# Kernel optimization log

Hardware: AMD Instinct MI355X
Metric: run time of the kernel (lower is better)

Reference implementation:

```python
import jax, jax.numpy as jnp
import numpy as np


def _ln(x, g, b, eps=1e-5):
    m = x.mean(-1, keepdims=True)
    v = ((x - m) ** 2).mean(-1, keepdims=True)
    return (x - m) * jax.lax.rsqrt(v + eps) * g + b


def setup_inputs() -> dict:
    key = jax.random.key(0)
    ks = jax.random.split(key, 12)
    B, S, I, H, E, P, O, EM = 32, 512, 64, 512, 8, 96, 64, 512
    D = S * I
    r = lambda k, shape, s=0.02: jax.random.normal(k, shape, jnp.float32) * s
    z = lambda *shape: jnp.zeros(shape, jnp.float32)
    o = lambda *shape: jnp.ones(shape, jnp.float32)
    return dict(
        x=jax.random.normal(ks[0], (B, S, I), jnp.float32),
        gW1=r(ks[1], (D, EM)), gb1=z(EM), gln1_g=o(EM), gln1_b=z(EM),
        gW2=r(ks[2], (EM, EM)), gb2=z(EM), gln2_g=o(EM), gln2_b=z(EM),
        gW3=r(ks[3], (EM, 128)), gb3=z(128),
        protos=jax.random.normal(ks[4], (E, 128), jnp.float32) * 0.01,
        temp=jnp.ones((), jnp.float32),
        eW1=r(ks[5], (E, I, H)), eb1=z(E, H),
        eW2=r(ks[6], (E, H, H)), eb2=z(E, H),
        fW1=r(ks[7], (H, H)), fb1=z(H), fln_g=o(H), fln_b=z(H),
        fW2=r(ks[8], (H, H)), fb2=z(H),
        ln_g=o(H), ln_b=z(H),
        pW1=r(ks[9], (H, H // 2)), pb1=z(H // 2), pln_g=o(H // 2), pln_b=z(H // 2),
        pW2=r(ks[10], (H // 2, P * O)), pb2=z(P * O),
        on_g=o(O), on_b=z(O),
    )


def reference(x, gW1, gb1, gln1_g, gln1_b, gW2, gb2, gln2_g, gln2_b, gW3, gb3,
              protos, temp, eW1, eb1, eW2, eb2,
              fW1, fb1, fln_g, fln_b, fW2, fb2, ln_g, ln_b,
              pW1, pb1, pln_g, pln_b, pW2, pb2, on_g, on_b):
    B, S, I = x.shape
    O = on_g.shape[0]
    P = pW2.shape[1] // O
    # 1) flow latent mapping (identity fallback path of the original code)
    x_flat = x.reshape(B, S * I)
    z_latent = x_flat
    # 2) gating encoder -> 128-d embedding (dropout = identity in eval)
    h = jax.nn.relu(_ln(z_latent @ gW1 + gb1, gln1_g, gln1_b))
    h = jax.nn.relu(_ln(h @ gW2 + gb2, gln2_g, gln2_b))
    emb = h @ gW3 + gb3  # [B, 128]
    # 3) routing: euclidean cdist to prototypes, temperature-scaled softmax
    d2 = jnp.sum((emb[:, None, :] - protos[None, :, :]) ** 2, axis=-1)
    dist = jnp.sqrt(jnp.maximum(d2, 1e-12))  # [B, E]
    t = jnp.clip(temp, 0.1, 5.0)
    w = jax.nn.softmax(-dist / t, axis=-1)  # [B, E]
    # 4) experts: per-expert FFN on raw input, all experts batched
    he = jax.nn.relu(jnp.einsum('bsi,eih->besh', x, eW1) + eb1[None, :, None, :])
    eo = jnp.einsum('besh,eho->beso', he, eW2) + eb2[None, :, None, :]  # [B,E,S,H]
    # 5) routing-weighted combine + fusion + prediction head
    fused = jnp.einsum('besh,be->bsh', eo, w)
    f = jax.nn.relu(_ln(fused @ fW1 + fb1, fln_g, fln_b)) @ fW2 + fb2
    f = _ln(f, ln_g, ln_b)
    last = f[:, -1, :]  # [B, H]
    p = jax.nn.relu(_ln(last @ pW1 + pb1, pln_g, pln_b)) @ pW2 + pb2
    p = p.reshape(B, P, O)
    return _ln(p, on_g, on_b)
```

## Files before the change

kernel.cpp:

```cpp
#include <hip/hip_runtime.h>
#include <math.h>

#define DIMK 32768

__device__ __forceinline__ void fma4(float4& a, float s, const float4 w) {
  a.x += s * w.x; a.y += s * w.y; a.z += s * w.z; a.w += s * w.w;
}

__device__ __forceinline__ float fsel(const float4& v, int kk) {
  return kk == 0 ? v.x : kk == 1 ? v.y : kk == 2 ? v.z : v.w;
}

__device__ __forceinline__ float wave_sum(float v) {
  v += __shfl_xor(v, 1); v += __shfl_xor(v, 2); v += __shfl_xor(v, 4);
  v += __shfl_xor(v, 8); v += __shfl_xor(v, 16); v += __shfl_xor(v, 32);
  return v;
}

__device__ __forceinline__ void gld_lds16(const float* g, float* l) {
  __builtin_amdgcn_global_load_lds(
      (const __attribute__((address_space(1))) void*)g,
      (__attribute__((address_space(3))) void*)l, 16, 0, 0);
}

__device__ __forceinline__ float block_sum(float v, float* red, int n) {
  int t = threadIdx.x;
  red[t] = v;
  __syncthreads();
  for (int s = n >> 1; s > 0; s >>= 1) {
    if (t < s) red[t] += red[t + s];
    __syncthreads();
  }
  float r = red[0];
  __syncthreads();
  return r;
}

__global__ __launch_bounds__(256) void gemm1(const float* __restrict__ x,
                                             const float* __restrict__ gW1,
                                             float* __restrict__ part) {
  const int mt = blockIdx.x, ks = blockIdx.y;
  const int m0 = mt * 128, k0 = ks * 256;
  const int t = threadIdx.x;
  __shared__ float As[32 * 256];
  __shared__ float Ws[2][32 * 128];

  const float* Wp = gW1 + (size_t)k0 * 512 + m0;

#pragma unroll
  for (int j = 0; j < 8; ++j) {
    int i = t + j * 256;
    gld_lds16(x + (size_t)(i >> 6) * DIMK + k0 + (i & 63) * 4, &As[i * 4]);
  }
#pragma unroll
  for (int j = 0; j < 4; ++j) {
    int i = t + j * 256;
    gld_lds16(Wp + (size_t)(i >> 5) * 512 + (i & 31) * 4, &Ws[0][i * 4]);
  }

  const int mf4 = (t & 31) * 4;
  const int bg = t >> 5;
  float4 acc[4];
#pragma unroll
  for (int j = 0; j < 4; ++j) acc[j] = make_float4(0.f, 0.f, 0.f, 0.f);
  const float* a0 = &As[bg * 4 * 256];

  for (int s = 0; s < 8; ++s) {
    __syncthreads();
    if (s < 7) {
      const float* Wn = Wp + (size_t)(s + 1) * 32 * 512;
#pragma unroll
      for (int j = 0; j < 4; ++j) {
        int i = t + j * 256;
        gld_lds16(Wn + (size_t)(i >> 5) * 512 + (i & 31) * 4, &Ws[(s + 1) & 1][i * 4]);
      }
    }
    const float* Wc = Ws[s & 1];
    const int sc = s * 32;
#pragma unroll
    for (int kq = 0; kq < 8; ++kq) {
      float4 av0 = *(const float4*)(a0 + sc + kq * 4);
      float4 av1 = *(const float4*)(a0 + 256 + sc + kq * 4);
      float4 av2 = *(const float4*)(a0 + 512 + sc + kq * 4);
      float4 av3 = *(const float4*)(a0 + 768 + sc + kq * 4);
#pragma unroll
      for (int kk = 0; kk < 4; ++kk) {
        float4 wv = *(const float4*)&Wc[(kq * 4 + kk) * 128 + mf4];
        fma4(acc[0], fsel(av0, kk), wv);
        fma4(acc[1], fsel(av1, kk), wv);
        fma4(acc[2], fsel(av2, kk), wv);
        fma4(acc[3], fsel(av3, kk), wv);
      }
    }
  }

  float* op = part + ((size_t)ks * 32 + bg * 4) * 512 + m0 + mf4;
#pragma unroll
  for (int j = 0; j < 4; ++j) *(float4*)(op + (size_t)j * 512) = acc[j];
}

__global__ __launch_bounds__(256) void pr_he(const float* __restrict__ part,
                                             float* __restrict__ pre,
                                             const float* __restrict__ x,
                                             const float* __restrict__ eW1,
                                             const float* __restrict__ eb1,
                                             float* __restrict__ he_all) {
  __shared__ float sm[18432];
  const int bid = blockIdx.x, t = threadIdx.x;
  if (bid < 256) {
    const int b = bid & 31, c = bid >> 5;
#pragma unroll
    for (int h = 0; h < 2; ++h) {
      int m = t + h * 256;
      float a = 0.f;
      const float* p = part + ((size_t)c * 16 * 32 + b) * 512 + m;
#pragma unroll
      for (int i = 0; i < 16; ++i) a += p[(size_t)i * 16384];
      pre[((size_t)c * 32 + b) * 512 + m] = a;
    }
  } else {
    const int idx = bid - 256;
    const int e = idx >> 1, hs = idx & 1;
    float* xs = sm;
    float* Ws = sm + 2048;
    for (int i = t; i < 512; i += 256) {
      int b = i >> 4, q = i & 15;
      *(float4*)&xs[b * 64 + q * 4] = *(const float4*)(x + (size_t)b * DIMK + 32704 + q * 4);
    }
    const float* w1 = eW1 + (size_t)e * 64 * 512 + hs * 256;
    for (int i = t; i < 64 * 64; i += 256) {
      int k = i >> 6, q = i & 63;
      *(float4*)&Ws[k * 256 + q * 4] = *(const float4*)(w1 + (size_t)k * 512 + q * 4);
    }
    __syncthreads();
    float acc[32];
#pragma unroll
    for (int b = 0; b < 32; ++b) acc[b] = 0.f;
#pragma unroll 4
    for (int k = 0; k < 64; ++k) {
      float wk = Ws[k * 256 + t];
#pragma unroll
      for (int b = 0; b < 32; ++b) acc[b] += xs[b * 64 + k] * wk;
    }
    float bb = eb1[e * 512 + hs * 256 + t];
    for (int b = 0; b < 32; ++b)
      he_all[((size_t)e * 32 + b) * 512 + hs * 256 + t] = fmaxf(acc[b] + bb, 0.f);
  }
}

__global__ __launch_bounds__(256) void ln_eg(const float* __restrict__ pre,
                                             const float* __restrict__ gb1,
                                             const float* __restrict__ g,
                                             const float* __restrict__ bt,
                                             float* __restrict__ h1,
                                             const float* __restrict__ he_all,
                                             const float* __restrict__ eW2,
                                             float* __restrict__ epart) {
  __shared__ float sm[6272];
  const int bid = blockIdx.x, t = threadIdx.x;
  if (bid < 32) {
    const int b = bid;
    float a0 = gb1[t], a1 = gb1[t + 256];
    for (int kq = 0; kq < 8; ++kq) {
      const float* p = pre + ((size_t)kq * 32 + b) * 512;
      a0 += p[t]; a1 += p[t + 256];
    }
    const int lane = t & 63, wid = t >> 6;
    float s = wave_sum(a0 + a1);
    if (lane == 0) sm[wid] = s;
    __syncthreads();
    float mean = (sm[0] + sm[1] + sm[2] + sm[3]) * (1.f / 512.f);
    float d0 = a0 - mean, d1 = a1 - mean;
    __syncthreads();
    float q = wave_sum(d0 * d0 + d1 * d1);
    if (lane == 0) sm[wid] = q;
    __syncthreads();
    float var = (sm[0] + sm[1] + sm[2] + sm[3]) * (1.f / 512.f);
    float rr = rsqrtf(var + 1e-5f);
    h1[b * 512 + t] = fmaxf(d0 * rr * g[t] + bt[t], 0.f);
    h1[b * 512 + t + 256] = fmaxf(d1 * rr * g[t + 256] + bt[t + 256], 0.f);
  } else {
    const int idx = bid - 32;
    const int mt = idx & 7, kq = (idx >> 3) & 7, e = idx >> 6;
    constexpr int KC = 64;
    float* Ws = sm;
    float* As = sm + KC * 64;
    const int m0 = mt * 64, k0 = kq * KC;
    const float* Wp = eW2 + (size_t)e * 512 * 512 + (size_t)k0 * 512 + m0;
    for (int i = t; i < KC * 16; i += 256) {
      int r = i >> 4, q = i & 15;
      *(float4*)&Ws[r * 64 + q * 4] = *(const float4*)(Wp + (size_t)r * 512 + q * 4);
    }
    const float* Ap = he_all + (size_t)e * 32 * 512 + k0;
    for (int i = t; i < 32 * (KC / 4); i += 256) {
      int b = i / (KC / 4), q = i % (KC / 4);
      *(float4*)&As[b * (KC + 4) + q * 4] = *(const float4*)(Ap + (size_t)b * 512 + q * 4);
    }
    __syncthreads();
    const int mf = t & 15, bg = t >> 4;
    const int b0 = bg * 2;
    float4 acc0 = make_float4(0.f, 0.f, 0.f, 0.f), acc1 = acc0;
    const float* a0 = &As[b0 * (KC + 4)];
    const float* a1 = &As[(b0 + 1) * (KC + 4)];
#pragma unroll 8
    for (int k = 0; k < KC; ++k) {
      float4 wv = *(const float4*)&Ws[k * 64 + mf * 4];
      fma4(acc0, a0[k], wv);
      fma4(acc1, a1[k], wv);
    }
    float* op = epart + ((size_t)(kq * 8 + e) * 32 + b0) * 512 + m0 + mf * 4;
    *(float4*)op = acc0;
    *(float4*)(op + 512) = acc1;
  }
}

template <int KC>
__global__ __launch_bounds__(256) void gemm_tile(const float* __restrict__ A,
                                                 const float* __restrict__ W,
                                                 float* __restrict__ outp,
                                                 int M, int aRow) {
  const int mt = blockIdx.x, kq = blockIdx.y;
  const int m0 = mt * 64, k0 = kq * KC;
  const int t = threadIdx.x;
  __shared__ float Ws[KC * 64];
  __shared__ float As[32 * (KC + 4)];
  const float* Wp = W + (size_t)k0 * M + m0;
  for (int i = t; i < KC * 16; i += 256) {
    int r = i >> 4, q = i & 15;
    *(float4*)&Ws[r * 64 + q * 4] = *(const float4*)(Wp + (size_t)r * M + q * 4);
  }
  const float* Ap = A + k0;
  for (int i = t; i < 32 * (KC / 4); i += 256) {
    int b = i / (KC / 4), q = i % (KC / 4);
    *(float4*)&As[b * (KC + 4) + q * 4] = *(const float4*)(Ap + (size_t)b * aRow + q * 4);
  }
  __syncthreads();
  const int mf = t & 15, bg = t >> 4;
  const int b0 = bg * 2;
  float4 acc0 = make_float4(0.f, 0.f, 0.f, 0.f), acc1 = acc0;
  const float* a0 = &As[b0 * (KC + 4)];
  const float* a1 = &As[(b0 + 1) * (KC + 4)];
#pragma unroll 8
  for (int k = 0; k < KC; ++k) {
    float4 wv = *(const float4*)&Ws[k * 64 + mf * 4];
    fma4(acc0, a0[k], wv);
    fma4(acc1, a1[k], wv);
  }
  float* op = outp + ((size_t)kq * 32 + b0) * M + m0 + mf * 4;
  *(float4*)op = acc0;
  *(float4*)(op + M) = acc1;
}

__global__ void red_ln(const float* __restrict__ zp, const float* __restrict__ bias,
                       const float* __restrict__ g, const float* __restrict__ bt,
                       float* __restrict__ outp, int M, int nq, int relu) {
  const int b = blockIdx.x, t = threadIdx.x;
  __shared__ float red[512];
  float a = bias[t];
#pragma unroll 4
  for (int kq = 0; kq < nq; ++kq) a += zp[((size_t)kq * 32 + b) * M + t];
  float fM = 1.f / (float)M;
  float mean = block_sum(a, red, M) * fM;
  float d = a - mean;
  float var = block_sum(d * d, red, M) * fM;
  float v = d * rsqrtf(var + 1e-5f) * g[t] + bt[t];
  outp[b * M + t] = relu ? fmaxf(v, 0.f) : v;
}

__global__ __launch_bounds__(512) void gate_mix(const float* __restrict__ zp,
                                                const float* __restrict__ gb2,
                                                const float* __restrict__ g2,
                                                const float* __restrict__ bt2,
                                                const float* __restrict__ gW3,
                                                const float* __restrict__ gb3,
                                                const float* __restrict__ protos,
                                                const float* __restrict__ temp,
                                                const float* __restrict__ epart,
                                                const float* __restrict__ eb2,
                                                float* __restrict__ fused) {
  const int b = blockIdx.x, t = threadIdx.x;
  __shared__ float red[512];
  __shared__ float Arow[512];
  __shared__ float pacc[16 * 128];
  __shared__ float emb[128];
  __shared__ float d2s[8];
  __shared__ float wl[8];

  float a = gb2[t];
#pragma unroll
  for (int kq = 0; kq < 8; ++kq) a += zp[((size_t)kq * 32 + b) * 512 + t];
  float mean = block_sum(a, red, 512) * (1.f / 512.f);
  float d = a - mean;
  float var = block_sum(d * d, red, 512) * (1.f / 512.f);
  Arow[t] = fmaxf(d * rsqrtf(var + 1e-5f) * g2[t] + bt2[t], 0.f);
  __syncthreads();

  const int m4 = (t & 31) * 4, kg = t >> 5;
  const float* Wp = gW3 + (size_t)kg * 32 * 128 + m4;
  float4 acc = make_float4(0.f, 0.f, 0.f, 0.f);
  const float* ar = &Arow[kg * 32];
#pragma unroll 8
  for (int k = 0; k < 32; ++k) {
    float4 wv = *(const float4*)(Wp + (size_t)k * 128);
    fma4(acc, ar[k], wv);
  }
  *(float4*)&pacc[kg * 128 + m4] = acc;
  __syncthreads();
  if (t < 128) {
    float e = gb3[t];
#pragma unroll
    for (int k2 = 0; k2 < 16; ++k2) e += pacc[k2 * 128 + t];
    emb[t] = e;
  }
  __syncthreads();

  const int lane = t & 63, wid = t >> 6;
  float dd0 = emb[lane] - protos[wid * 128 + lane];
  float dd1 = emb[lane + 64] - protos[wid * 128 + 64 + lane];
  float q = wave_sum(dd0 * dd0 + dd1 * dd1);
  if (lane == 0) d2s[wid] = q;
  __syncthreads();
  if (t == 0) {
    float tt = fminf(fmaxf(temp[0], 0.1f), 5.0f);
    float lg[8], mx = -1e30f;
#pragma unroll
    for (int e = 0; e < 8; ++e) {
      float dist = sqrtf(fmaxf(d2s[e], 1e-12f));
      lg[e] = -dist / tt;
      mx = fmaxf(mx, lg[e]);
    }
    float se = 0.f;
#pragma unroll
    for (int e = 0; e < 8; ++e) { lg[e] = expf(lg[e] - mx); se += lg[e]; }
#pragma unroll
    for (int e = 0; e < 8; ++e) wl[e] = lg[e] / se;
  }
  __syncthreads();

  float fa = 0.f;
#pragma unroll
  for (int e = 0; e < 8; ++e) {
    float s = eb2[e * 512 + t];
#pragma unroll
    for (int kq = 0; kq < 8; ++kq)
      s += epart[(((size_t)kq * 8 + e) * 32 + b) * 512 + t];
    fa += wl[e] * s;
  }
  fused[b * 512 + t] = fa;
}

__global__ __launch_bounds__(256) void fin_red(const float* __restrict__ fpart,
                                               const float* __restrict__ pb2,
                                               const float* __restrict__ ong,
                                               const float* __restrict__ onb,
                                               float* __restrict__ outp) {
  const int t = threadIdx.x;
  const int lane = t & 63, w = t >> 6;
  const int r = blockIdx.x * 4 + w;
  const int b = r / 96, pi = r % 96;
  const int m = pi * 64 + lane;
  float a = pb2[m];
#pragma unroll
  for (int kq = 0; kq < 4; ++kq) a += fpart[((size_t)kq * 32 + b) * 6144 + m];
  float s = wave_sum(a);
  float mean = s * (1.f / 64.f);
  float d = a - mean;
  float q = wave_sum(d * d);
  float rr = rsqrtf(q * (1.f / 64.f) + 1e-5f);
  outp[((size_t)b * 96 + pi) * 64 + lane] = d * rr * ong[lane] + onb[lane];
}

extern "C" void kernel_launch(void* const* d_in, const int* in_sizes, int n_in,
                              void* d_out, int out_size, void* d_ws, size_t ws_size,
                              hipStream_t stream) {
  (void)in_sizes; (void)n_in; (void)out_size; (void)ws_size;
  const float* x      = (const float*)d_in[0];
  const float* gW1    = (const float*)d_in[1];
  const float* gb1    = (const float*)d_in[2];
  const float* gln1_g = (const float*)d_in[3];
  const float* gln1_b = (const float*)d_in[4];
  const float* gW2    = (const float*)d_in[5];
  const float* gb2    = (const float*)d_in[6];
  const float* gln2_g = (const float*)d_in[7];
  const float* gln2_b = (const float*)d_in[8];
  const float* gW3    = (const float*)d_in[9];
  const float* gb3    = (const float*)d_in[10];
  const float* protos = (const float*)d_in[11];
  const float* temp   = (const float*)d_in[12];
  const float* eW1    = (const float*)d_in[13];
  const float* eb1    = (const float*)d_in[14];
  const float* eW2    = (const float*)d_in[15];
  const float* eb2    = (const float*)d_in[16];
  const float* fW1    = (const float*)d_in[17];
  const float* fb1    = (const float*)d_in[18];
  const float* fln_g  = (const float*)d_in[19];
  const float* fln_b  = (const float*)d_in[20];
  const float* fW2    = (const float*)d_in[21];
  const float* fb2    = (const float*)d_in[22];
  const float* ln_g   = (const float*)d_in[23];
  const float* ln_b   = (const float*)d_in[24];
  const float* pW1    = (const float*)d_in[25];
  const float* pb1    = (const float*)d_in[26];
  const float* pln_g  = (const float*)d_in[27];
  const float* pln_b  = (const float*)d_in[28];
  const float* pW2    = (const float*)d_in[29];
  const float* pb2    = (const float*)d_in[30];
  const float* on_g   = (const float*)d_in[31];
  const float* on_b   = (const float*)d_in[32];
  float* out = (float*)d_out;

  float* ws     = (float*)d_ws;
  float* part   = ws;
  float* epart  = ws;
  float* he_all = ws + 1048576;
  float* fpart  = ws;
  float* h1     = ws + 2097152;
  float* zp     = h1 + 16384;
  float* fused  = zp + 262144;
  float* f1     = fused + 16384;
  float* lastv  = f1 + 16384;
  float* pp     = lastv + 16384;

  gemm1<<<dim3(4, 128), 256, 0, stream>>>(x, gW1, part);
  pr_he<<<272, 256, 0, stream>>>(part, zp, x, eW1, eb1, he_all);
  ln_eg<<<544, 256, 0, stream>>>(zp, gb1, gln1_g, gln1_b, h1, he_all, eW2, epart);
  gemm_tile<64><<<dim3(8, 8), 256, 0, stream>>>(h1, gW2, zp, 512, 512);
  gate_mix<<<32, 512, 0, stream>>>(zp, gb2, gln2_g, gln2_b, gW3, gb3, protos,
                                   temp, epart, eb2, fused);
  gemm_tile<64><<<dim3(8, 8), 256, 0, stream>>>(fused, fW1, zp, 512, 512);
  red_ln<<<32, 512, 0, stream>>>(zp, fb1, fln_g, fln_b, f1, 512, 8, 1);
  gemm_tile<64><<<dim3(8, 8), 256, 0, stream>>>(f1, fW2, zp, 512, 512);
  red_ln<<<32, 512, 0, stream>>>(zp, fb2, ln_g, ln_b, lastv, 512, 8, 0);
  gemm_tile<64><<<dim3(4, 8), 256, 0, stream>>>(lastv, pW1, zp, 256, 512);
  red_ln<<<32, 256, 0, stream>>>(zp, pb1, pln_g, pln_b, pp, 256, 8, 1);
  gemm_tile<64><<<dim3(96, 4), 256, 0, stream>>>(pp, pW2, fpart, 6144, 256);
  fin_red<<<768, 256, 0, stream>>>(fpart, pb2, on_g, on_b, out);
}
```

Before: 273.1 us.

## Split gate_mix into 4 column chunks per batch and use wave-level reductions

Replaces the tree-based shared-memory block_sum in red_ln with wave shuffles plus a small per-wave cross-sum, cutting the number of barriers. The gate/mix kernel is relaunched as a 32x4 grid of 128-thread blocks. Each block redundantly recomputes the LN, the gW3 projection and the softmax routing, then handles only a 128-column slice of the expert combine. This spreads the heavy epart read across four times more blocks, at the cost of repeating the gating work four times with a serial 512-length dot per thread.

Result: slower. 293.4 us (+7.4%).

```diff
diff --git a/kernel.cpp b/kernel.cpp
--- a/kernel.cpp
+++ b/kernel.cpp
@@ -17,23 +17,16 @@
   return v;
 }
 
+__device__ __forceinline__ float group16_sum(float v) {
+  v += __shfl_xor(v, 1); v += __shfl_xor(v, 2);
+  v += __shfl_xor(v, 4); v += __shfl_xor(v, 8);
+  return v;
+}
+
 __device__ __forceinline__ void gld_lds16(const float* g, float* l) {
   __builtin_amdgcn_global_load_lds(
       (const __attribute__((address_space(1))) void*)g,
       (__attribute__((address_space(3))) void*)l, 16, 0, 0);
-}
-
-__device__ __forceinline__ float block_sum(float v, float* red, int n) {
-  int t = threadIdx.x;
-  red[t] = v;
-  __syncthreads();
-  for (int s = n >> 1; s > 0; s >>= 1) {
-    if (t < s) red[t] += red[t + s];
-    __syncthreads();
-  }
-  float r = red[0];
-  __syncthreads();
-  return r;
 }
 
 __global__ __launch_bounds__(256) void gemm1(const float* __restrict__ x,
@@ -255,70 +248,98 @@
                        const float* __restrict__ g, const float* __restrict__ bt,
                        float* __restrict__ outp, int M, int nq, int relu) {
   const int b = blockIdx.x, t = threadIdx.x;
-  __shared__ float red[512];
+  __shared__ float red[8];
+  const int nw = M >> 6;
   float a = bias[t];
 #pragma unroll 4
   for (int kq = 0; kq < nq; ++kq) a += zp[((size_t)kq * 32 + b) * M + t];
+  const int lane = t & 63, wid = t >> 6;
   float fM = 1.f / (float)M;
-  float mean = block_sum(a, red, M) * fM;
+  float s = wave_sum(a);
+  if (lane == 0) red[wid] = s;
+  __syncthreads();
+  float tot = 0.f;
+  for (int w = 0; w < nw; ++w) tot += red[w];
+  float mean = tot * fM;
   float d = a - mean;
-  float var = block_sum(d * d, red, M) * fM;
+  __syncthreads();
+  float q = wave_sum(d * d);
+  if (lane == 0) red[wid] = q;
+  __syncthreads();
+  float tv = 0.f;
+  for (int w = 0; w < nw; ++w) tv += red[w];
+  float var = tv * fM;
   float v = d * rsqrtf(var + 1e-5f) * g[t] + bt[t];
   outp[b * M + t] = relu ? fmaxf(v, 0.f) : v;
 }
 
-__global__ __launch_bounds__(512) void gate_mix(const float* __restrict__ zp,
-                                                const float* __restrict__ gb2,
-                                                const float* __restrict__ g2,
-                                                const float* __restrict__ bt2,
-                                                const float* __restrict__ gW3,
-                                                const float* __restrict__ gb3,
-                                                const float* __restrict__ protos,
-                                                const float* __restrict__ temp,
-                                                const float* __restrict__ epart,
-                                                const float* __restrict__ eb2,
-                                                float* __restrict__ fused) {
-  const int b = blockIdx.x, t = threadIdx.x;
-  __shared__ float red[512];
+__global__ __launch_bounds__(128) void ffuse_gate(const float* __restrict__ zp,
+                                                  const float* __restrict__ gb2,
+                                                  const float* __restrict__ g2,
+                                                  const float* __restrict__ bt2,
+                                                  const float* __restrict__ gW3,
+                                                  const float* __restrict__ gb3,
+                                                  const float* __restrict__ protos,
+                                                  const float* __restrict__ temp,
+                                                  const float* __restrict__ epart,
+                                                  const float* __restrict__ eb2,
+                                                  float* __restrict__ fused) {
+  const int b = blockIdx.x, ch = blockIdx.y, t = threadIdx.x;
   __shared__ float Arow[512];
-  __shared__ float pacc[16 * 128];
   __shared__ float emb[128];
+  __shared__ float red2[2];
   __shared__ float d2s[8];
   __shared__ float wl[8];
 
-  float a = gb2[t];
-#pragma unroll
-  for (int kq = 0; kq < 8; ++kq) a += zp[((size_t)kq * 32 + b) * 512 + t];
-  float mean = block_sum(a, red, 512) * (1.f / 512.f);
-  float d = a - mean;
-  float var = block_sum(d * d, red, 512) * (1.f / 512.f);
-  Arow[t] = fmaxf(d * rsqrtf(var + 1e-5f) * g2[t] + bt2[t], 0.f);
-  __syncthreads();
-
-  const int m4 = (t & 31) * 4, kg = t >> 5;
-  const float* Wp = gW3 + (size_t)kg * 32 * 128 + m4;
-  float4 acc = make_float4(0.f, 0.f, 0.f, 0.f);
-  const float* ar = &Arow[kg * 32];
+  float a[4];
+#pragma unroll
+  for (int j = 0; j < 4; ++j) {
+    int m = t + j * 128;
+    float v = gb2[m];
+#pragma unroll
+    for (int kq = 0; kq < 8; ++kq) v += zp[((size_t)kq * 32 + b) * 512 + m];
+    a[j] = v;
+  }
+  const int lane = t & 63, wid = t >> 6;
+  float s = wave_sum(a[0] + a[1] + a[2] + a[3]);
+  if (lane == 0) red2[wid] = s;
+  __syncthreads();
+  float mean = (red2[0] + red2[1]) * (1.f / 512.f);
+  float q = 0.f;
+#pragma unroll
+  for (int j = 0; j < 4; ++j) { float d = a[j] - mean; q += d * d; }
+  __syncthreads();
+  q = wave_sum(q);
+  if (lane == 0) red2[wid] = q;
+  __syncthreads();
+  float rr = rsqrtf((red2[0] + red2[1]) * (1.f / 512.f) + 1e-5f);
+#pragma unroll
+  for (int j = 0; j < 4; ++j) {
+    int m = t + j * 128;
+    Arow[m] = fmaxf((a[j] - mean) * rr * g2[m] + bt2[m], 0.f);
+  }
+  __syncthreads();
+
+  {
+    float e = gb3[t];
 #pragma unroll 8
-  for (int k = 0; k < 32; ++k) {
-    float4 wv = *(const float4*)(Wp + (size_t)k * 128);
-    fma4(acc, ar[k], wv);
-  }
-  *(float4*)&pacc[kg * 128 + m4] = acc;
-  __syncthreads();
-  if (t < 128) {
-    float e = gb3[t];
-#pragma unroll
-    for (int k2 = 0; k2 < 16; ++k2) e += pacc[k2 * 128 + t];
+    for (int k = 0; k < 512; ++k) e += Arow[k] * gW3[(size_t)k * 128 + t];
     emb[t] = e;
   }
   __syncthreads();
 
-  const int lane = t & 63, wid = t >> 6;
-  float dd0 = emb[lane] - protos[wid * 128 + lane];
-  float dd1 = emb[lane + 64] - protos[wid * 128 + 64 + lane];
-  float q = wave_sum(dd0 * dd0 + dd1 * dd1);
-  if (lane == 0) d2s[wid] = q;
+  {
+    const int e = t >> 4, l16 = t & 15;
+    float qq = 0.f;
+#pragma unroll
+    for (int j = 0; j < 8; ++j) {
+      int dix = l16 + j * 16;
+      float dd = emb[dix] - protos[e * 128 + dix];
+      qq += dd * dd;
+    }
+    qq = group16_sum(qq);
+    if (l16 == 0) d2s[e] = qq;
+  }
   __syncthreads();
   if (t == 0) {
     float tt = fminf(fmaxf(temp[0], 0.1f), 5.0f);
@@ -337,16 +358,17 @@
   }
   __syncthreads();
 
+  const int m = ch * 128 + t;
   float fa = 0.f;
 #pragma unroll
   for (int e = 0; e < 8; ++e) {
-    float s = eb2[e * 512 + t];
+    float se = eb2[e * 512 + m];
 #pragma unroll
     for (int kq = 0; kq < 8; ++kq)
-      s += epart[(((size_t)kq * 8 + e) * 32 + b) * 512 + t];
-    fa += wl[e] * s;
-  }
-  fused[b * 512 + t] = fa;
+      se += epart[(((size_t)kq * 8 + e) * 32 + b) * 512 + m];
+    fa += wl[e] * se;
+  }
+  fused[b * 512 + m] = fa;
 }
 
 __global__ __launch_bounds__(256) void fin_red(const float* __restrict__ fpart,
@@ -425,8 +447,8 @@
   pr_he<<<272, 256, 0, stream>>>(part, zp, x, eW1, eb1, he_all);
   ln_eg<<<544, 256, 0, stream>>>(zp, gb1, gln1_g, gln1_b, h1, he_all, eW2, epart);
   gemm_tile<64><<<dim3(8, 8), 256, 0, stream>>>(h1, gW2, zp, 512, 512);
-  gate_mix<<<32, 512, 0, stream>>>(zp, gb2, gln2_g, gln2_b, gW3, gb3, protos,
-                                   temp, epart, eb2, fused);
+  ffuse_gate<<<dim3(32, 4), 128, 0, stream>>>(zp, gb2, gln2_g, gln2_b, gW3, gb3,
+                                              protos, temp, epart, eb2, fused);
   gemm_tile<64><<<dim3(8, 8), 256, 0, stream>>>(fused, fW1, zp, 512, 512);
   red_ln<<<32, 512, 0, stream>>>(zp, fb1, fln_g, fln_b, f1, 512, 8, 1);
   gemm_tile<64><<<dim3(8, 8), 256, 0, stream>>>(f1, fW2, zp, 512, 512);
```
